# Optimization experiments

Hardware: AMD Instinct MI355X
Metric: run time of the kernel (lower is better)

Reference implementation:

```python
import jax, jax.numpy as jnp
import numpy as np

B, D, C = 8192, 2048, 1000
EPS32 = float(np.finfo(np.float32).eps)      # torch clamp_probs uses finfo.eps
LOG_2PI = float(np.log(2.0 * np.pi))
GAMMA = float(1.0 / np.exp(100.0))           # lerp at global_step=0 -> start_val = 1/exp(start_rho)


def setup_inputs() -> dict:
    key = jax.random.key(0)
    k = jax.random.split(key, 6)
    feature = jax.random.normal(k[0], (B, D), jnp.float32)
    target = jax.random.randint(k[1], (B,), 0, C)
    eps = jax.random.normal(k[2], (B, D), jnp.float32)
    # y_project: Linear(C, D) -> weight [D, C], bias [D]
    y_w = jax.random.normal(k[3], (D, C), jnp.float32) * 0.02
    y_b = jnp.zeros((D,), jnp.float32)
    # cls_project: Linear(D, C) -> weight [C, D], bias [C]
    # small weights + positive bias keep Categorical probs positive (torch would
    # clamp negatives to eps; we replicate the clamp but avoid degenerate NaNs)
    cls_w = jax.random.normal(k[4], (C, D), jnp.float32) * 0.001
    cls_b = jnp.ones((C,), jnp.float32) * 5.0
    return dict(feature=feature, y_w=y_w, y_b=y_b, cls_w=cls_w, cls_b=cls_b,
                eps=eps, target=target)


def reference(feature, y_w, y_b, cls_w, cls_b, eps, target):
    # z = m.sample() : identity-covariance MVN sample, detached (torch .sample())
    z = jax.lax.stop_gradient(feature + eps)                      # [B, D]

    # y_emb = y_project(one_hot(target)) == gather of weight columns + bias
    y_emb = jnp.take(y_w, target, axis=1).T + y_b                 # [B, D]

    # Categorical(probs=cls_project(z)): normalize, clamp, log
    probs_raw = z @ cls_w.T + cls_b                               # [B, C]
    p = probs_raw / jnp.sum(probs_raw, axis=-1, keepdims=True)
    logits = jnp.log(jnp.clip(p, EPS32, 1.0 - EPS32))             # [B, C]

    # identity-covariance MVN log_prob in closed form
    const = 0.5 * D * LOG_2PI
    h1 = 0.5 * jnp.sum((z - feature) ** 2, axis=-1) + const       # -m.log_prob(z)
    h2 = 0.5 * jnp.sum((z - y_emb) ** 2, axis=-1) + const         # -y_emb_d.log_prob(z)
    h3 = -jnp.take_along_axis(logits, target[:, None], axis=1)[:, 0]

    rex = h2 - h1
    loss = jnp.mean(jnp.float32(GAMMA) * rex + h3)
    return logits, loss
```

## Files before the change

### kernel.cpp

```cpp
#include <hip/hip_runtime.h>
#include <hip/hip_bf16.h>

#define B_ROWS 8192
#define D_DIM  2048
#define C_DIM  1000
#define C_PAD  1024

#define EPS32   1.1920928955078125e-07f

typedef __attribute__((ext_vector_type(8))) short short8;
typedef __attribute__((ext_vector_type(4))) float f32x4;

#define GLOAD_LDS16(gptr, lptr) \
  __builtin_amdgcn_global_load_lds((const __attribute__((address_space(1))) void*)(gptr), \
                                   (__attribute__((address_space(3))) void*)(lptr), 16, 0, 0)

__device__ inline unsigned short f2bf(float x) {
  union { __hip_bfloat16 b; unsigned short u; } cv;
  cv.b = __float2bfloat16(x);
  return cv.u;
}

__device__ inline float wave_red(float v) {
#pragma unroll
  for (int off = 32; off > 0; off >>= 1) v += __shfl_down(v, off, 64);
  return v;
}

__global__ __launch_bounds__(256) void fuse_z(const float4* __restrict__ f4,
                                              const float4* __restrict__ e4,
                                              uint2* __restrict__ z,
                                              const float* __restrict__ cls_w,
                                              __hip_bfloat16* __restrict__ clsw_bf) {
  int bid = blockIdx.x;
  if (bid < 16384) {
    int i = bid * 256 + threadIdx.x;
    float4 f = f4[i];
    float4 e = e4[i];
    union { unsigned short u[4]; uint2 v; } pz;
    pz.u[0] = f2bf(f.x + e.x);
    pz.u[1] = f2bf(f.y + e.y);
    pz.u[2] = f2bf(f.z + e.z);
    pz.u[3] = f2bf(f.w + e.w);
    z[i] = pz.v;
  } else {
    int j = ((bid - 16384) * 256 + threadIdx.x) * 8;
    int row = j >> 11;
    int col = j & 2047;
    union { unsigned short u[8]; uint4 v; } pk;
    if (row < C_DIM) {
      const float* src = cls_w + (size_t)row * D_DIM + col;
#pragma unroll
      for (int i2 = 0; i2 < 8; ++i2) pk.u[i2] = f2bf(src[i2]);
    } else {
#pragma unroll
      for (int i2 = 0; i2 < 8; ++i2) pk.u[i2] = 0;
    }
    *(uint4*)((unsigned short*)clsw_bf + j) = pk.v;
  }
}

__global__ __launch_bounds__(256) void gemm_bt(const __hip_bfloat16* __restrict__ A,
                                               const __hip_bfloat16* __restrict__ Bt,
                                               const float* __restrict__ cls_b,
                                               float* __restrict__ out) {
  __shared__ __align__(16) __hip_bfloat16 sA[128 * 64];
  __shared__ __align__(16) __hip_bfloat16 sB[128 * 64];
  const int tid = threadIdx.x;
  const int m0 = blockIdx.x * 128;
  const int n0 = blockIdx.y * 128;
  const int w = tid >> 6, lane = tid & 63;
  const int wm = (w & 1) * 64, wn = (w >> 1) * 64;
  const int l15 = lane & 15, quad = lane >> 4;

  f32x4 acc[4][4] = {};

  for (int k0 = 0; k0 < D_DIM; k0 += 64) {
#pragma unroll
    for (int i = 0; i < 4; ++i) {
      int j = i * 256 + tid;
      int row = j >> 3;
      int cc = (j & 7) ^ (row & 7);
      const __hip_bfloat16* srcA = A + (size_t)(m0 + row) * D_DIM + k0 + cc * 8;
      const __hip_bfloat16* srcB = Bt + (size_t)(n0 + row) * D_DIM + k0 + cc * 8;
      GLOAD_LDS16(srcA, &sA[j * 8]);
      GLOAD_LDS16(srcB, &sB[j * 8]);
    }
    __syncthreads();
#pragma unroll
    for (int kk = 0; kk < 64; kk += 32) {
      const int ccr = (kk >> 3) + quad;
      short8 af[4], bfr[4];
#pragma unroll
      for (int i = 0; i < 4; ++i) {
        int r = wm + i * 16 + l15;
        af[i] = *(const short8*)&sA[(r * 8 + (ccr ^ (r & 7))) * 8];
      }
#pragma unroll
      for (int jn = 0; jn < 4; ++jn) {
        int r = wn + jn * 16 + l15;
        bfr[jn] = *(const short8*)&sB[(r * 8 + (ccr ^ (r & 7))) * 8];
      }
#pragma unroll
      for (int i = 0; i < 4; ++i)
#pragma unroll
        for (int jn = 0; jn < 4; ++jn)
          acc[i][jn] = __builtin_amdgcn_mfma_f32_16x16x32_bf16(af[i], bfr[jn], acc[i][jn], 0, 0, 0);
    }
    __syncthreads();
  }

#pragma unroll
  for (int i = 0; i < 4; ++i) {
    int row = m0 + wm + i * 16 + quad * 4;
#pragma unroll
    for (int jn = 0; jn < 4; ++jn) {
      int col = n0 + wn + jn * 16 + l15;
      if (col < C_DIM) {
        float bias = cls_b[col];
#pragma unroll
        for (int r = 0; r < 4; ++r)
          out[(size_t)(row + r) * C_DIM + col] = acc[i][jn][r] + bias;
      }
    }
  }
}

__global__ __launch_bounds__(256) void rownorm(float* __restrict__ out,
                                               const int* __restrict__ target,
                                               float* __restrict__ rowloss) {
  int b = blockIdx.x * 4 + (threadIdx.x >> 6);
  int lane = threadIdx.x & 63;
  float* row = out + (size_t)b * C_DIM;

  float v[16];
  float s = 0.f;
#pragma unroll
  for (int k = 0; k < 4; ++k) {
    int c = k * 256 + lane * 4;
    if (c + 3 < C_DIM) {
      float4 f = *(const float4*)(row + c);
      v[k * 4 + 0] = f.x; v[k * 4 + 1] = f.y; v[k * 4 + 2] = f.z; v[k * 4 + 3] = f.w;
    } else {
#pragma unroll
      for (int i = 0; i < 4; ++i) v[k * 4 + i] = (c + i < C_DIM) ? row[c + i] : 0.f;
    }
    s += v[k * 4 + 0] + v[k * 4 + 1] + v[k * 4 + 2] + v[k * 4 + 3];
  }
  s = wave_red(s);
  float inv = 1.0f / __shfl(s, 0, 64);
  int t = target[b];

#pragma unroll
  for (int k = 0; k < 4; ++k) {
    int c = k * 256 + lane * 4;
    float lg[4];
#pragma unroll
    for (int i = 0; i < 4; ++i) {
      float p = v[k * 4 + i] * inv;
      p = fminf(fmaxf(p, EPS32), 1.0f - EPS32);
      lg[i] = __logf(p);
      if (c + i == t) rowloss[b] = -lg[i];
    }
    if (c + 3 < C_DIM) {
      *(float4*)(row + c) = make_float4(lg[0], lg[1], lg[2], lg[3]);
    } else {
#pragma unroll
      for (int i = 0; i < 4; ++i) if (c + i < C_DIM) row[c + i] = lg[i];
    }
  }
}

__global__ __launch_bounds__(256) void finalize(const float* __restrict__ rowloss,
                                                float* __restrict__ out_loss) {
  int tid = threadIdx.x;
  float s = 0.f;
  for (int i = tid; i < B_ROWS; i += 256) s += rowloss[i];
  s = wave_red(s);
  __shared__ float sm[4];
  if ((tid & 63) == 0) sm[tid >> 6] = s;
  __syncthreads();
  if (tid == 0) out_loss[0] = (sm[0] + sm[1] + sm[2] + sm[3]) * (1.0f / B_ROWS);
}

extern "C" void kernel_launch(void* const* d_in, const int* in_sizes, int n_in,
                              void* d_out, int out_size, void* d_ws, size_t ws_size,
                              hipStream_t stream) {
  const float* feature = (const float*)d_in[0];
  const float* cls_w   = (const float*)d_in[3];
  const float* cls_b   = (const float*)d_in[4];
  const float* eps     = (const float*)d_in[5];
  const int*   target  = (const int*)d_in[6];
  float* out = (float*)d_out;
  float* out_loss = out + (size_t)B_ROWS * C_DIM;

  char* ws = (char*)d_ws;
  __hip_bfloat16* z_bf    = (__hip_bfloat16*)ws;
  __hip_bfloat16* clsw_bf = (__hip_bfloat16*)(ws + 33554432);
  float*          rowloss = (float*)(ws + 33554432 + 4194304);

  fuse_z<<<dim3(16384 + 1024), 256, 0, stream>>>((const float4*)feature, (const float4*)eps,
                                                 (uint2*)z_bf, cls_w, clsw_bf);
  gemm_bt<<<dim3(B_ROWS / 128, C_PAD / 128), 256, 0, stream>>>(z_bf, clsw_bf, cls_b, out);
  rownorm<<<dim3(B_ROWS / 4), 256, 0, stream>>>(out, target, rowloss);
  finalize<<<dim3(1), 256, 0, stream>>>(rowloss, out_loss);
}
```

Measured before the change: 239.3 us.

## Fuse feature+eps add and bf16 cast into GEMM A-tile loading

Removes the separate pass that materialized z in bf16, and instead loads fp32 feature and eps inside the GEMM, adds them and converts them into the LDS A tile. The weight cast becomes its own small kernel. This avoids writing and re-reading the z intermediate and one launch. The cost is that every N-tile block re-reads fp32 activations (8x redundant traffic at double width), and A loads stop using direct global-to-LDS transfers.

```diff
diff --git a/kernel.cpp b/kernel.cpp
--- a/kernel.cpp
+++ b/kernel.cpp
@@ -27,40 +27,25 @@
   return v;
 }
 
-__global__ __launch_bounds__(256) void fuse_z(const float4* __restrict__ f4,
-                                              const float4* __restrict__ e4,
-                                              uint2* __restrict__ z,
-                                              const float* __restrict__ cls_w,
+__global__ __launch_bounds__(256) void cast_w(const float* __restrict__ cls_w,
                                               __hip_bfloat16* __restrict__ clsw_bf) {
-  int bid = blockIdx.x;
-  if (bid < 16384) {
-    int i = bid * 256 + threadIdx.x;
-    float4 f = f4[i];
-    float4 e = e4[i];
-    union { unsigned short u[4]; uint2 v; } pz;
-    pz.u[0] = f2bf(f.x + e.x);
-    pz.u[1] = f2bf(f.y + e.y);
-    pz.u[2] = f2bf(f.z + e.z);
-    pz.u[3] = f2bf(f.w + e.w);
-    z[i] = pz.v;
+  int j = (blockIdx.x * 256 + threadIdx.x) * 8;
+  int row = j >> 11;
+  int col = j & 2047;
+  union { unsigned short u[8]; uint4 v; } pk;
+  if (row < C_DIM) {
+    const float* src = cls_w + (size_t)row * D_DIM + col;
+#pragma unroll
+    for (int i2 = 0; i2 < 8; ++i2) pk.u[i2] = f2bf(src[i2]);
   } else {
-    int j = ((bid - 16384) * 256 + threadIdx.x) * 8;
-    int row = j >> 11;
-    int col = j & 2047;
-    union { unsigned short u[8]; uint4 v; } pk;
-    if (row < C_DIM) {
-      const float* src = cls_w + (size_t)row * D_DIM + col;
-#pragma unroll
-      for (int i2 = 0; i2 < 8; ++i2) pk.u[i2] = f2bf(src[i2]);
-    } else {
-#pragma unroll
-      for (int i2 = 0; i2 < 8; ++i2) pk.u[i2] = 0;
-    }
-    *(uint4*)((unsigned short*)clsw_bf + j) = pk.v;
-  }
-}
-
-__global__ __launch_bounds__(256) void gemm_bt(const __hip_bfloat16* __restrict__ A,
+#pragma unroll
+    for (int i2 = 0; i2 < 8; ++i2) pk.u[i2] = 0;
+  }
+  *(uint4*)((unsigned short*)clsw_bf + j) = pk.v;
+}
+
+__global__ __launch_bounds__(256) void gemm_fz(const float* __restrict__ feature,
+                                               const float* __restrict__ eps,
                                                const __hip_bfloat16* __restrict__ Bt,
                                                const float* __restrict__ cls_b,
                                                float* __restrict__ out) {
@@ -76,15 +61,40 @@
   f32x4 acc[4][4] = {};
 
   for (int k0 = 0; k0 < D_DIM; k0 += 64) {
+    float4 fa[4], fb[4], ea[4], eb[4];
 #pragma unroll
     for (int i = 0; i < 4; ++i) {
       int j = i * 256 + tid;
       int row = j >> 3;
       int cc = (j & 7) ^ (row & 7);
-      const __hip_bfloat16* srcA = A + (size_t)(m0 + row) * D_DIM + k0 + cc * 8;
+      const float* sF = feature + (size_t)(m0 + row) * D_DIM + k0 + cc * 8;
+      const float* sE = eps     + (size_t)(m0 + row) * D_DIM + k0 + cc * 8;
+      fa[i] = *(const float4*)sF;
+      fb[i] = *(const float4*)(sF + 4);
+      ea[i] = *(const float4*)sE;
+      eb[i] = *(const float4*)(sE + 4);
+    }
+#pragma unroll
+    for (int i = 0; i < 4; ++i) {
+      int j = i * 256 + tid;
+      int row = j >> 3;
+      int cc = (j & 7) ^ (row & 7);
       const __hip_bfloat16* srcB = Bt + (size_t)(n0 + row) * D_DIM + k0 + cc * 8;
-      GLOAD_LDS16(srcA, &sA[j * 8]);
       GLOAD_LDS16(srcB, &sB[j * 8]);
+    }
+#pragma unroll
+    for (int i = 0; i < 4; ++i) {
+      int j = i * 256 + tid;
+      union { unsigned short u[8]; uint4 v; } pk;
+      pk.u[0] = f2bf(fa[i].x + ea[i].x);
+      pk.u[1] = f2bf(fa[i].y + ea[i].y);
+      pk.u[2] = f2bf(fa[i].z + ea[i].z);
+      pk.u[3] = f2bf(fa[i].w + ea[i].w);
+      pk.u[4] = f2bf(fb[i].x + eb[i].x);
+      pk.u[5] = f2bf(fb[i].y + eb[i].y);
+      pk.u[6] = f2bf(fb[i].z + eb[i].z);
+      pk.u[7] = f2bf(fb[i].w + eb[i].w);
+      *(uint4*)&sA[j * 8] = pk.v;
     }
     __syncthreads();
 #pragma unroll
@@ -195,13 +205,11 @@
   float* out_loss = out + (size_t)B_ROWS * C_DIM;
 
   char* ws = (char*)d_ws;
-  __hip_bfloat16* z_bf    = (__hip_bfloat16*)ws;
-  __hip_bfloat16* clsw_bf = (__hip_bfloat16*)(ws + 33554432);
-  float*          rowloss = (float*)(ws + 33554432 + 4194304);
-
-  fuse_z<<<dim3(16384 + 1024), 256, 0, stream>>>((const float4*)feature, (const float4*)eps,
-                                                 (uint2*)z_bf, cls_w, clsw_bf);
-  gemm_bt<<<dim3(B_ROWS / 128, C_PAD / 128), 256, 0, stream>>>(z_bf, clsw_bf, cls_b, out);
+  __hip_bfloat16* clsw_bf = (__hip_bfloat16*)ws;
+  float*          rowloss = (float*)(ws + 4194304);
+
+  cast_w<<<dim3(1024), 256, 0, stream>>>(cls_w, clsw_bf);
+  gemm_fz<<<dim3(B_ROWS / 128, C_PAD / 128), 256, 0, stream>>>(feature, eps, clsw_bf, cls_b, out);
   rownorm<<<dim3(B_ROWS / 4), 256, 0, stream>>>(out, target, rowloss);
   finalize<<<dim3(1), 256, 0, stream>>>(rowloss, out_loss);
 }
```

Result: slower. 270.6 us (+13.1%).
